# Optimization experiments

Hardware: AMD Instinct MI355X
Metric: run time of the kernel (lower is better)

## Reference

```python
import jax, jax.numpy as jnp
import numpy as np

B, N, D = 2, 4096, 1024
DS = 1024           # state_dim (defaults to embed_dim)
H = 4096            # mlp hidden = int(embed_dim * 4.0)
EPS = 1e-5


def _layernorm(x, w, b):
    mu = jnp.mean(x, axis=-1, keepdims=True)
    var = jnp.mean((x - mu) ** 2, axis=-1, keepdims=True)
    return (x - mu) * jax.lax.rsqrt(var + EPS) * w + b


def _selective_scan(deltaA, deltaB_u):
    # deltaA: (B, N, 1), deltaB_u: (B, N, DS). Recurrence h_i = dA_i * h + dBu_i.
    def step(h, inp):
        dA, dBu = inp           # (B,1), (B,DS)
        h = dA * h + dBu
        return h, h
    h0 = jnp.zeros((deltaB_u.shape[0], deltaB_u.shape[2]), deltaB_u.dtype)
    _, ys = jax.lax.scan(step, h0,
                         (jnp.swapaxes(deltaA, 0, 1), jnp.swapaxes(deltaB_u, 0, 1)))
    return jnp.swapaxes(ys, 0, 1)   # (B, N, DS)


def _forward(x, norm1_w, norm1_b, gate_w, gate_b, state_w, state_b,
             out_w, out_b, norm2_w, norm2_b, mlp_w1, mlp_b1, mlp_w2, mlp_b2):
    xn = _layernorm(x, norm1_w, norm1_b)
    g = xn @ gate_w + gate_b                       # (B,N,2D)
    gate, gate_gate = jnp.split(g, 2, axis=-1)
    gate = jax.nn.silu(gate)
    gate_gate = jax.nn.silu(gate_gate)
    u = (xn * gate) @ state_w + state_b            # (B,N,DS)
    Bm = gate_gate @ state_w + state_b             # (B,N,DS)
    # A = -ones(DS) -> delta*A = -delta broadcast over DS; keep (B,N,1)
    delta = jax.nn.softplus(jnp.mean(xn @ state_w + state_b, axis=-1, keepdims=True))
    deltaA = jnp.exp(-delta)                       # (B,N,1)
    deltaB_u = delta * Bm * u                      # (B,N,DS)
    # C = ones -> y_i = C_i * h_i = h_i
    y = _selective_scan(deltaA, deltaB_u)
    ssm_out = y @ out_w + out_b
    x = x + ssm_out
    x2 = _layernorm(x, norm2_w, norm2_b)
    mlp = jax.nn.gelu(x2 @ mlp_w1 + mlp_b1, approximate=False) @ mlp_w2 + mlp_b2
    return x + mlp


def setup_inputs() -> dict:
    key = jax.random.key(0)
    ks = jax.random.split(key, 12)
    s = 0.02
    p = lambda k, shape: jax.random.normal(k, shape, jnp.float32) * s
    return {
        "x": jax.random.normal(ks[0], (B, N, D), jnp.float32),
        "norm1_w": jnp.ones((D,), jnp.float32), "norm1_b": jnp.zeros((D,), jnp.float32),
        "gate_w": p(ks[1], (D, 2 * D)), "gate_b": p(ks[2], (2 * D,)),
        "state_w": p(ks[3], (D, DS)), "state_b": p(ks[4], (DS,)),
        "out_w": p(ks[5], (DS, D)), "out_b": p(ks[6], (D,)),
        "norm2_w": jnp.ones((D,), jnp.float32), "norm2_b": jnp.zeros((D,), jnp.float32),
        "mlp_w1": p(ks[7], (D, H)), "mlp_b1": p(ks[8], (H,)),
        "mlp_w2": p(ks[9], (H, D)), "mlp_b2": p(ks[10], (D,)),
    }


def reference(x, norm1_w, norm1_b, gate_w, gate_b, state_w, state_b,
              out_w, out_b, norm2_w, norm2_b, mlp_w1, mlp_b1, mlp_w2, mlp_b2):
    return _forward(x, norm1_w, norm1_b, gate_w, gate_b, state_w, state_b,
                    out_w, out_b, norm2_w, norm2_b, mlp_w1, mlp_b1, mlp_w2, mlp_b2)
```

## Files before the change

kernel.cpp:

```cpp
#include <hip/hip_runtime.h>
#include <hip/hip_bf16.h>
#include <math.h>

#define B_   2
#define N_   4096
#define D_   1024
#define DS_  1024
#define HID_ 4096
#define ROWS (B_ * N_)

#define CHK 128
#define TCH 32

typedef __attribute__((ext_vector_type(8))) short bf16x8;
typedef __attribute__((ext_vector_type(4))) float f32x4;

#define ASG __attribute__((address_space(1)))
#define AS3 __attribute__((address_space(3)))

__device__ __forceinline__ float bf2f(unsigned short u) {
  union { float f; unsigned int i; } v; v.i = ((unsigned int)u) << 16; return v.f;
}
__device__ __forceinline__ unsigned short f2bf(float f) {
  union { float f; unsigned int i; } v; v.f = f;
  unsigned int r = v.i + 0x7fffu + ((v.i >> 16) & 1u);
  return (unsigned short)(r >> 16);
}

__global__ void means_kernel(const float* __restrict__ W, const float* __restrict__ bvec,
                             float* __restrict__ swmean, float* __restrict__ sbmean) {
  __shared__ float sm[4];
  int bid = blockIdx.x, t = threadIdx.x;
  const float* src = (bid < D_) ? (W + (size_t)bid * DS_) : bvec;
  float s = 0.f;
  for (int j = t; j < DS_; j += 256) s += src[j];
  for (int o = 32; o; o >>= 1) s += __shfl_down(s, o);
  if ((t & 63) == 0) sm[t >> 6] = s;
  __syncthreads();
  if (t == 0) {
    float r = (sm[0] + sm[1] + sm[2] + sm[3]) * (1.f / DS_);
    if (bid < D_) swmean[bid] = r; else sbmean[0] = r;
  }
}

__global__ void transpose_all_kernel(const float* __restrict__ gw, const float* __restrict__ sw,
                                     const float* __restrict__ ow, const float* __restrict__ w1,
                                     const float* __restrict__ w2,
                                     unsigned short* __restrict__ gwT, unsigned short* __restrict__ swT,
                                     unsigned short* __restrict__ owT, unsigned short* __restrict__ w1T,
                                     unsigned short* __restrict__ w2T) {
  __shared__ float tile[32][33];
  int b = blockIdx.x;
  const float* W; unsigned short* WT; int K, N, t0;
  if (b < 2048)      { W = gw; WT = gwT; K = 1024; N = 2048; t0 = b; }
  else if (b < 3072) { W = sw; WT = swT; K = 1024; N = 1024; t0 = b - 2048; }
  else if (b < 4096) { W = ow; WT = owT; K = 1024; N = 1024; t0 = b - 3072; }
  else if (b < 8192) { W = w1; WT = w1T; K = 1024; N = 4096; t0 = b - 4096; }
  else               { W = w2; WT = w2T; K = 4096; N = 1024; t0 = b - 8192; }
  int ntx = N >> 5;
  int bn = (t0 % ntx) * 32, bk = (t0 / ntx) * 32;
  int tx = threadIdx.x & 31, ty = threadIdx.x >> 5;
  for (int i = ty; i < 32; i += 8)
    tile[i][tx] = W[(size_t)(bk + i) * N + bn + tx];
  __syncthreads();
  for (int i = ty; i < 32; i += 8)
    WT[(size_t)(bn + i) * K + bk + tx] = f2bf(tile[tx][i]);
}

template<bool WITH_DELTA, bool BF16IN>
__global__ void ln_kernel(const void* __restrict__ xin, const float* __restrict__ w,
                          const float* __restrict__ bb, unsigned short* __restrict__ out_bf,
                          const float* __restrict__ swmean, const float* __restrict__ sbmean,
                          float* __restrict__ delta, float* __restrict__ ea) {
  __shared__ float sm[8];
  __shared__ float bc[2];
  int row = blockIdx.x, t = threadIdx.x;
  float x0, x1, x2, x3;
  if (BF16IN) {
    const unsigned short* xr = (const unsigned short*)xin + (size_t)row * D_;
    ushort4 xv = ((const ushort4*)xr)[t];
    x0 = bf2f(xv.x); x1 = bf2f(xv.y); x2 = bf2f(xv.z); x3 = bf2f(xv.w);
  } else {
    const float* xr = (const float*)xin + (size_t)row * D_;
    float4 xv = ((const float4*)xr)[t];
    x0 = xv.x; x1 = xv.y; x2 = xv.z; x3 = xv.w;
  }
  float s  = x0 + x1 + x2 + x3;
  float sq = x0 * x0 + x1 * x1 + x2 * x2 + x3 * x3;
  for (int o = 32; o; o >>= 1) { s += __shfl_down(s, o); sq += __shfl_down(sq, o); }
  if ((t & 63) == 0) { sm[t >> 6] = s; sm[4 + (t >> 6)] = sq; }
  __syncthreads();
  if (t == 0) {
    float ts = sm[0] + sm[1] + sm[2] + sm[3];
    float tq = sm[4] + sm[5] + sm[6] + sm[7];
    float mu = ts * (1.f / D_);
    float var = tq * (1.f / D_) - mu * mu;
    bc[0] = mu; bc[1] = rsqrtf(var + 1e-5f);
  }
  __syncthreads();
  float mu = bc[0], rs = bc[1];
  float4 wv = ((const float4*)w)[t];
  float4 bv = ((const float4*)bb)[t];
  float n0 = (x0 - mu) * rs * wv.x + bv.x;
  float n1 = (x1 - mu) * rs * wv.y + bv.y;
  float n2 = (x2 - mu) * rs * wv.z + bv.z;
  float n3 = (x3 - mu) * rs * wv.w + bv.w;
  ushort4 o4; o4.x = f2bf(n0); o4.y = f2bf(n1); o4.z = f2bf(n2); o4.w = f2bf(n3);
  ((ushort4*)(out_bf + (size_t)row * D_))[t] = o4;
  if (WITH_DELTA) {
    float4 sw = ((const float4*)swmean)[t];
    float d = n0 * sw.x + n1 * sw.y + n2 * sw.z + n3 * sw.w;
    for (int o = 32; o; o >>= 1) d += __shfl_down(d, o);
    if ((t & 63) == 0) sm[t >> 6] = d;
    __syncthreads();
    if (t == 0) {
      float z = sm[0] + sm[1] + sm[2] + sm[3] + sbmean[0];
      float dl = (z > 15.f) ? z : log1pf(__expf(z));
      delta[row] = dl;
      ea[row] = __expf(-dl);
    }
  }
}


#define BARX { __builtin_amdgcn_s_barrier(); __builtin_amdgcn_sched_barrier(0); }

#define RD_A(TAU, H) { const char* ab_ = smem + ((((TAU)&1)*2+(H))<<14); \
  _Pragma("unroll") for (int mm_ = 0; mm_ < MB_H; ++mm_) \
  _Pragma("unroll") for (int ks_ = 0; ks_ < 2; ++ks_) { \
    int r_ = wr*(16*MB_H) + mm_*16 + l15; \
    int by_ = r_*128 + ks_*64 + kq16; by_ ^= ((by_>>7)&7)<<4; \
    af[mm_][ks_] = *(const bf16x8*)(ab_ + by_); } }

#define RD_B(TAU, H, DST) { const char* bb_ = smemB + ((((TAU)&1)*2+(H)))*SB; \
  _Pragma("unroll") for (int nn_ = 0; nn_ < NB_H; ++nn_) \
  _Pragma("unroll") for (int ks_ = 0; ks_ < 2; ++ks_) { \
    int r_ = wc*(16*NB_H) + nn_*16 + l15; \
    int by_ = r_*128 + ks_*64 + kq16; by_ ^= ((by_>>7)&7)<<4; \
    DST[nn_][ks_] = *(const bf16x8*)(bb_ + by_); } }

#define MFMAQ(QA, QB, BF) { __builtin_amdgcn_s_setprio(1); \
  _Pragma("unroll") for (int m_ = 0; m_ < MB_H; ++m_) \
  _Pragma("unroll") for (int n_ = 0; n_ < NB_H; ++n_) \
  _Pragma("unroll") for (int k_ = 0; k_ < 2; ++k_) \
    acc[(QA)*MB_H+m_][(QB)*NB_H+n_] = __builtin_amdgcn_mfma_f32_16x16x32_bf16( \
        af[m_][k_], BF[n_][k_], acc[(QA)*MB_H+m_][(QB)*NB_H+n_], 0, 0, 0); \
  __builtin_amdgcn_s_setprio(0); }

template<int EPI>
__device__ __forceinline__ void epi_store(float v, size_t off, void* Cout, const float* res) {
  if (EPI == 1) {
    v = v / (1.f + __expf(-v));
    ((unsigned short*)Cout)[off] = f2bf(v);
  } else if (EPI == 2) {
    ((unsigned short*)Cout)[off] = f2bf(v);
  } else if (EPI == 3) {
    ((float*)Cout)[off] = v + res[off];
  } else if (EPI == 4) {
    float tt = v * (0.7978845608f + 0.0356774081f * v * v);
    v = v / (1.f + __expf(-2.f * tt));
    ((unsigned short*)Cout)[off] = f2bf(v);
  } else if (EPI == 6) {
    ((unsigned short*)Cout)[off] = f2bf(v + res[off]);
  } else if (EPI == 7) {
    ((float*)Cout)[off] = v + bf2f(((const unsigned short*)res)[off]);
  }
}

template<int BN, int EPI>
__global__ __launch_bounds__(512, 2) void gemm8p(
    const unsigned short* __restrict__ A1p, int lda1, int M1,
    const unsigned short* __restrict__ A2p, int lda2,
    const unsigned short* __restrict__ BT, const float* __restrict__ bias,
    void* __restrict__ Cout, const float* __restrict__ res,
    int N, int K, int nbx) {
  constexpr int WN   = (BN == 256) ? 4 : 2;
  constexpr int MB_H = (BN == 256) ? 4 : 2;
  constexpr int NB_H = 2;
  constexpr int MF   = 2 * MB_H;
  constexpr int LB   = BN / 128;
  constexpr int SB   = (BN / 2) * 64 * 2;
  __shared__ char smem[65536 + 4 * SB];
  char* smemB = smem + 65536;

  const int nwg = gridDim.x;
  int bid = blockIdx.x;
  int wg = (bid & 7) * (nwg >> 3) + (bid >> 3);
  const int bx = wg % nbx, by = wg / nbx;
  const int mbase = by * 256, nbase = bx * BN;

  const int tid = threadIdx.x;
  const int lane = tid & 63, wid = tid >> 6;
  const int wr = wid / WN, wc = wid % WN;
  const int l15 = lane & 15, kq16 = (lane >> 4) * 16;
  const int wvoff16 = wid << 10;

  const unsigned short* Ause; int ldaU;
  if (mbase < M1) { Ause = A1p + (size_t)mbase * lda1; ldaU = lda1; }
  else            { Ause = A2p + (size_t)(mbase - M1) * lda2; ldaU = lda2; }

  int L0 = tid * 16;        int b0 = L0 ^ (((L0 >> 7) & 7) << 4);
  int L1 = 8192 + tid * 16; int b1 = L1 ^ (((L1 >> 7) & 7) << 4);
  const unsigned short* pA0 = Ause + (size_t)(b0 >> 7) * ldaU + ((b0 & 127) >> 1);
  const unsigned short* pA1 = Ause + (size_t)(b1 >> 7) * ldaU + ((b1 & 127) >> 1);
  const unsigned short* pB0 = BT + (size_t)(nbase + (b0 >> 7)) * K + ((b0 & 127) >> 1);
  const unsigned short* pB1 = BT + (size_t)(nbase + (b1 >> 7)) * K + ((b1 & 127) >> 1);

  auto stageA = [&](int tau, int h, bool en) {
    if (!en) return;
    char* l0 = smem + (((tau & 1) * 2 + h) << 14) + wvoff16;
    const unsigned short* g0 = pA0 + (size_t)h * 128 * ldaU + tau * 64;
    const unsigned short* g1 = pA1 + (size_t)h * 128 * ldaU + tau * 64;
    __builtin_amdgcn_global_load_lds((const ASG void*)g0, (AS3 void*)l0, 16, 0, 0);
    __builtin_amdgcn_global_load_lds((const ASG void*)g1, (AS3 void*)(l0 + 8192), 16, 0, 0);
  };
  auto stageB = [&](int tau, int h, bool en) {
    if (!en) return;
    char* l0 = smemB + ((tau & 1) * 2 + h) * SB + wvoff16;
    const unsigned short* g0 = pB0 + (size_t)h * (BN / 2) * K + tau * 64;
    __builtin_amdgcn_global_load_lds((const ASG void*)g0, (AS3 void*)l0, 16, 0, 0);
    if constexpr (LB == 2) {
      const unsigned short* g1 = pB1 + (size_t)h * (BN / 2) * K + tau * 64;
      __builtin_amdgcn_global_load_lds((const ASG void*)g1, (AS3 void*)(l0 + 8192), 16, 0, 0);
    }
  };
  auto vm_steady = [&]() {
    if constexpr (BN == 256) { asm volatile("s_waitcnt vmcnt(6)" ::: "memory"); }
    else                     { asm volatile("s_waitcnt vmcnt(5)" ::: "memory"); }
  };

  f32x4 acc[MF][4];
#pragma unroll
  for (int m = 0; m < MF; ++m)
#pragma unroll
    for (int n = 0; n < 4; ++n) acc[m][n] = (f32x4){0.f, 0.f, 0.f, 0.f};
  bf16x8 af[MB_H][2], bq0[NB_H][2], bq1[NB_H][2];

  const int NT = K >> 6, NI = NT >> 1;

  stageA(0, 0, true); stageB(0, 0, true); stageA(0, 1, true); stageB(0, 1, true);
  stageA(1, 0, true); stageB(1, 0, true); stageA(1, 1, true);
  vm_steady();
  BARX;

#pragma unroll 1
  for (int i = 0; i < NI; ++i) {
    const int t0 = 2 * i;
    const bool st = (i < NI - 1);
    stageB(t0 + 1, 1, true); RD_A(t0, 0); RD_B(t0, 0, bq0);
    BARX; MFMAQ(0, 0, bq0); BARX;
    stageA(t0 + 2, 0, st); RD_B(t0, 1, bq1);
    BARX; MFMAQ(0, 1, bq1); BARX;
    stageB(t0 + 2, 0, st); RD_A(t0, 1);
    BARX; MFMAQ(1, 1, bq1); BARX;
    stageA(t0 + 2, 1, st);
    if (st) { vm_steady(); } else { asm volatile("s_waitcnt vmcnt(0)" ::: "memory"); }
    BARX; MFMAQ(1, 0, bq0); BARX;
    stageB(t0 + 2, 1, st); RD_A(t0 + 1, 0); RD_B(t0 + 1, 0, bq0);
    BARX; MFMAQ(0, 0, bq0); BARX;
    stageA(t0 + 3, 0, st); RD_B(t0 + 1, 1, bq1);
    BARX; MFMAQ(0, 1, bq1); BARX;
    stageB(t0 + 3, 0, st); RD_A(t0 + 1, 1);
    BARX; MFMAQ(1, 1, bq1); BARX;
    stageA(t0 + 3, 1, st);
    if (st) vm_steady();
    BARX; MFMAQ(1, 0, bq0); BARX;
  }

  const int r0 = (lane >> 4) * 4;
#pragma unroll
  for (int mb = 0; mb < MF; ++mb) {
    int row = mbase + wr * (16 * MB_H) + (mb % MB_H) * 16 + (mb / MB_H) * 128 + r0;
#pragma unroll
    for (int nb = 0; nb < 4; ++nb) {
      int col = nbase + wc * (16 * NB_H) + (nb % NB_H) * 16 + (nb / NB_H) * (BN / 2) + l15;
      float bc = bias[col];
#pragma unroll
      for (int r = 0; r < 4; ++r)
        epi_store<EPI>(acc[mb][nb][r] + bc, (size_t)(row + r) * N + col, Cout, res);
    }
  }
}

__global__ void ew_xg_kernel(const unsigned short* __restrict__ xn,
                             const unsigned short* __restrict__ gs,
                             unsigned short* __restrict__ xg) {
  size_t i8 = ((size_t)blockIdx.x * 256 + threadIdx.x) * 8;
  size_t row = i8 >> 10, col = i8 & 1023;
  uint4 xv = *(const uint4*)(xn + i8);
  uint4 gv = *(const uint4*)(gs + row * 2048 + col);
  const unsigned short* xs = (const unsigned short*)&xv;
  const unsigned short* gg = (const unsigned short*)&gv;
  uint4 ov; unsigned short* o = (unsigned short*)&ov;
#pragma unroll
  for (int j = 0; j < 8; ++j) o[j] = f2bf(bf2f(xs[j]) * bf2f(gg[j]));
  *(uint4*)(xg + i8) = ov;
}

__global__ void scan_a_kernel(const unsigned short* __restrict__ u,
                              const unsigned short* __restrict__ bm,
                              const float* __restrict__ delta,
                              const float* __restrict__ ea,
                              float* __restrict__ hend, float* __restrict__ P) {
  int blk = blockIdx.x;
  int b = blk / CHK, c = blk % CHK;
  int ch = threadIdx.x;
  size_t base = ((size_t)(b * N_ + c * TCH)) * DS_ + ch;
  const float* dp = delta + b * N_ + c * TCH;
  const float* ep = ea + b * N_ + c * TCH;
  float h = 0.f, pa = 1.f;
#pragma unroll 4
  for (int t = 0; t < TCH; ++t) {
    float dl = dp[t], e = ep[t];
    float du = dl * bf2f(u[base + (size_t)t * DS_]) * bf2f(bm[base + (size_t)t * DS_]);
    h = e * h + du;
    pa *= e;
  }
  hend[(size_t)blk * DS_ + ch] = h;
  if (ch == 0) P[blk] = pa;
}

__global__ void scan_combine_kernel(const float* __restrict__ hend, const float* __restrict__ P,
                                    float* __restrict__ carryin) {
  int b = blockIdx.x >> 2;
  int ch = (blockIdx.x & 3) * 256 + threadIdx.x;
  float carry = 0.f;
  for (int c = 0; c < CHK; ++c) {
    size_t o = (size_t)(b * CHK + c) * DS_ + ch;
    carryin[o] = carry;
    carry = P[b * CHK + c] * carry + hend[o];
  }
}

__global__ void scan_b_kernel(const unsigned short* __restrict__ u,
                              const unsigned short* __restrict__ bm,
                              const float* __restrict__ delta,
                              const float* __restrict__ ea,
                              const float* __restrict__ carryin,
                              unsigned short* __restrict__ y) {
  int blk = blockIdx.x;
  int b = blk / CHK, c = blk % CHK;
  int ch = threadIdx.x;
  size_t base = ((size_t)(b * N_ + c * TCH)) * DS_ + ch;
  const float* dp = delta + b * N_ + c * TCH;
  const float* ep = ea + b * N_ + c * TCH;
  float h = carryin[(size_t)blk * DS_ + ch];
#pragma unroll 4
  for (int t = 0; t < TCH; ++t) {
    float dl = dp[t], e = ep[t];
    float du = dl * bf2f(u[base + (size_t)t * DS_]) * bf2f(bm[base + (size_t)t * DS_]);
    h = e * h + du;
    y[base + (size_t)t * DS_] = f2bf(h);
  }
}

extern "C" void kernel_launch(void* const* d_in, const int* in_sizes, int n_in,
                              void* d_out, int out_size, void* d_ws, size_t ws_size,
                              hipStream_t stream) {
  const float* x       = (const float*)d_in[0];
  const float* n1w     = (const float*)d_in[1];
  const float* n1b     = (const float*)d_in[2];
  const float* gate_w  = (const float*)d_in[3];
  const float* gate_b  = (const float*)d_in[4];
  const float* state_w = (const float*)d_in[5];
  const float* state_b = (const float*)d_in[6];
  const float* out_w   = (const float*)d_in[7];
  const float* out_b   = (const float*)d_in[8];
  const float* n2w     = (const float*)d_in[9];
  const float* n2b     = (const float*)d_in[10];
  const float* mlp_w1  = (const float*)d_in[11];
  const float* mlp_b1  = (const float*)d_in[12];
  const float* mlp_w2  = (const float*)d_in[13];
  const float* mlp_b2  = (const float*)d_in[14];
  float* outp = (float*)d_out;

  char* w = (char*)d_ws;
  size_t off = 0;
  auto alloc = [&](size_t bytes) { char* p = w + off; off += (bytes + 255) & ~(size_t)255; return p; };

  unsigned short* gate_wT  = (unsigned short*)alloc((size_t)2048 * 1024 * 2);
  unsigned short* state_wT = (unsigned short*)alloc((size_t)1024 * 1024 * 2);
  unsigned short* out_wT   = (unsigned short*)alloc((size_t)1024 * 1024 * 2);
  unsigned short* w1T      = (unsigned short*)alloc((size_t)4096 * 1024 * 2);
  unsigned short* w2T      = (unsigned short*)alloc((size_t)1024 * 4096 * 2);
  float* swmean  = (float*)alloc(D_ * 4);
  float* sbmean  = (float*)alloc(256);
  float* delta   = (float*)alloc((size_t)ROWS * 4);
  float* eadel   = (float*)alloc((size_t)ROWS * 4);
  float* hend    = (float*)alloc((size_t)B_ * CHK * DS_ * 4);
  float* carryin = (float*)alloc((size_t)B_ * CHK * DS_ * 4);
  float* P       = (float*)alloc((size_t)B_ * CHK * 4);
  unsigned short* xn = (unsigned short*)alloc((size_t)ROWS * D_ * 2);
  unsigned short* gs = (unsigned short*)alloc((size_t)ROWS * HID_ * 2);
  unsigned short* xg = (unsigned short*)alloc((size_t)ROWS * D_ * 2);
  float* x1f         = (float*)alloc((size_t)ROWS * D_ * 4);

  unsigned short* h1  = gs;
  unsigned short* y   = xg;
  unsigned short* x2  = xg;
  unsigned short* u   = (unsigned short*)x1f;
  unsigned short* bm  = u + (size_t)ROWS * D_;
  unsigned short* x1b = u;

  means_kernel<<<D_ + 1, 256, 0, stream>>>(state_w, state_b, swmean, sbmean);
  transpose_all_kernel<<<12288, 256, 0, stream>>>(gate_w, state_w, out_w, mlp_w1, mlp_w2,
                                                  gate_wT, state_wT, out_wT, w1T, w2T);

  ln_kernel<true, false><<<ROWS, 256, 0, stream>>>(x, n1w, n1b, xn, swmean, sbmean, delta, eadel);

  const int BIG = 1 << 30;
  gemm8p<256, 1><<<256, 512, 0, stream>>>(xn, 1024, BIG, xn, 1024,
                                          gate_wT, gate_b, gs, nullptr, 2048, 1024, 8);
  ew_xg_kernel<<<(ROWS * D_) / 8 / 256, 256, 0, stream>>>(xn, gs, xg);
  gemm8p<256, 2><<<256, 512, 0, stream>>>(xg, 1024, 8192, gs + 1024, 2048,
                                          state_wT, state_b, u, nullptr, 1024, 1024, 4);

  scan_a_kernel<<<B_ * CHK, 1024, 0, stream>>>(u, bm, delta, eadel, hend, P);
  scan_combine_kernel<<<B_ * 4, 256, 0, stream>>>(hend, P, carryin);
  scan_b_kernel<<<B_ * CHK, 1024, 0, stream>>>(u, bm, delta, eadel, carryin, y);

  gemm8p<128, 6><<<256, 512, 0, stream>>>(y, 1024, BIG, y, 1024,
                                          out_wT, out_b, x1b, x, 1024, 1024, 8);
  ln_kernel<false, true><<<ROWS, 256, 0, stream>>>(x1b, n2w, n2b, x2, nullptr, nullptr, nullptr, nullptr);
  gemm8p<256, 4><<<512, 512, 0, stream>>>(x2, 1024, BIG, x2, 1024,
                                          w1T, mlp_b1, h1, nullptr, 4096, 1024, 16);
  gemm8p<128, 7><<<256, 512, 0, stream>>>(h1, 4096, BIG, h1, 4096,
                                          w2T, mlp_b2, outp, (const float*)x1b, 1024, 4096, 8);
}
```

Baseline: 351.1 us.

## Fuse delta*Bm*u into state GEMM epilogue via interleaved row layout

The gate GEMM epilogue now applies SiLU and writes gate_gate directly into odd rows of an interleaved A buffer, while the elementwise kernel writes xn*gate into the even rows. The state GEMM then runs over this interleaved 2*ROWS matrix, and its epilogue pairs adjacent rows to emit delta*u*Bm straight as a bf16 tensor. The scan kernels read one precomputed tensor instead of u, Bm and delta, which removes a full read stream and the separate u/Bm stores. This relies on each thread's four accumulator rows being consecutive and aligned so that row pairs land in the same thread. Precision changes slightly because the product is rounded to bf16 before the scan.

```diff
diff --git a/kernel.cpp b/kernel.cpp
--- a/kernel.cpp
+++ b/kernel.cpp
@@ -173,7 +173,7 @@
     const unsigned short* __restrict__ A2p, int lda2,
     const unsigned short* __restrict__ BT, const float* __restrict__ bias,
     void* __restrict__ Cout, const float* __restrict__ res,
-    int N, int K, int nbx) {
+    int N, int K, int nbx, void* __restrict__ Cout2) {
   constexpr int WN   = (BN == 256) ? 4 : 2;
   constexpr int MB_H = (BN == 256) ? 4 : 2;
   constexpr int NB_H = 2;
@@ -275,45 +275,61 @@
     for (int nb = 0; nb < 4; ++nb) {
       int col = nbase + wc * (16 * NB_H) + (nb % NB_H) * 16 + (nb / NB_H) * (BN / 2) + l15;
       float bc = bias[col];
-#pragma unroll
-      for (int r = 0; r < 4; ++r)
-        epi_store<EPI>(acc[mb][nb][r] + bc, (size_t)(row + r) * N + col, Cout, res);
+      if (EPI == 9) {
+#pragma unroll
+        for (int pr = 0; pr < 2; ++pr) {
+          float e0 = acc[mb][nb][2 * pr] + bc;
+          float e1 = acc[mb][nb][2 * pr + 1] + bc;
+          int i0 = (row >> 1) + pr;
+          ((unsigned short*)Cout)[(size_t)i0 * N + col] = f2bf(res[i0] * e0 * e1);
+        }
+      } else if (EPI == 8) {
+#pragma unroll
+        for (int r = 0; r < 4; ++r) {
+          float v = acc[mb][nb][r] + bc;
+          v = v / (1.f + __expf(-v));
+          if (col < 1024)
+            ((unsigned short*)Cout)[(size_t)(row + r) * 1024 + col] = f2bf(v);
+          else
+            ((unsigned short*)Cout2)[(size_t)(2 * (row + r) + 1) * 1024 + (col - 1024)] = f2bf(v);
+        }
+      } else {
+#pragma unroll
+        for (int r = 0; r < 4; ++r)
+          epi_store<EPI>(acc[mb][nb][r] + bc, (size_t)(row + r) * N + col, Cout, res);
+      }
     }
   }
 }
 
 __global__ void ew_xg_kernel(const unsigned short* __restrict__ xn,
-                             const unsigned short* __restrict__ gs,
-                             unsigned short* __restrict__ xg) {
+                             const unsigned short* __restrict__ gs1,
+                             unsigned short* __restrict__ AI) {
   size_t i8 = ((size_t)blockIdx.x * 256 + threadIdx.x) * 8;
   size_t row = i8 >> 10, col = i8 & 1023;
   uint4 xv = *(const uint4*)(xn + i8);
-  uint4 gv = *(const uint4*)(gs + row * 2048 + col);
+  uint4 gv = *(const uint4*)(gs1 + i8);
   const unsigned short* xs = (const unsigned short*)&xv;
   const unsigned short* gg = (const unsigned short*)&gv;
   uint4 ov; unsigned short* o = (unsigned short*)&ov;
 #pragma unroll
   for (int j = 0; j < 8; ++j) o[j] = f2bf(bf2f(xs[j]) * bf2f(gg[j]));
-  *(uint4*)(xg + i8) = ov;
-}
-
-__global__ void scan_a_kernel(const unsigned short* __restrict__ u,
-                              const unsigned short* __restrict__ bm,
-                              const float* __restrict__ delta,
+  *(uint4*)(AI + ((row * 2) << 10) + col) = ov;
+}
+
+__global__ void scan_a_kernel(const unsigned short* __restrict__ dbu,
                               const float* __restrict__ ea,
                               float* __restrict__ hend, float* __restrict__ P) {
   int blk = blockIdx.x;
   int b = blk / CHK, c = blk % CHK;
   int ch = threadIdx.x;
   size_t base = ((size_t)(b * N_ + c * TCH)) * DS_ + ch;
-  const float* dp = delta + b * N_ + c * TCH;
   const float* ep = ea + b * N_ + c * TCH;
   float h = 0.f, pa = 1.f;
 #pragma unroll 4
   for (int t = 0; t < TCH; ++t) {
-    float dl = dp[t], e = ep[t];
-    float du = dl * bf2f(u[base + (size_t)t * DS_]) * bf2f(bm[base + (size_t)t * DS_]);
-    h = e * h + du;
+    float e = ep[t];
+    h = e * h + bf2f(dbu[base + (size_t)t * DS_]);
     pa *= e;
   }
   hend[(size_t)blk * DS_ + ch] = h;
@@ -332,9 +348,7 @@
   }
 }
 
-__global__ void scan_b_kernel(const unsigned short* __restrict__ u,
-                              const unsigned short* __restrict__ bm,
-                              const float* __restrict__ delta,
+__global__ void scan_b_kernel(const unsigned short* __restrict__ dbu,
                               const float* __restrict__ ea,
                               const float* __restrict__ carryin,
                               unsigned short* __restrict__ y) {
@@ -342,14 +356,12 @@
   int b = blk / CHK, c = blk % CHK;
   int ch = threadIdx.x;
   size_t base = ((size_t)(b * N_ + c * TCH)) * DS_ + ch;
-  const float* dp = delta + b * N_ + c * TCH;
   const float* ep = ea + b * N_ + c * TCH;
   float h = carryin[(size_t)blk * DS_ + ch];
 #pragma unroll 4
   for (int t = 0; t < TCH; ++t) {
-    float dl = dp[t], e = ep[t];
-    float du = dl * bf2f(u[base + (size_t)t * DS_]) * bf2f(bm[base + (size_t)t * DS_]);
-    h = e * h + du;
+    float e = ep[t];
+    h = e * h + bf2f(dbu[base + (size_t)t * DS_]);
     y[base + (size_t)t * DS_] = f2bf(h);
   }
 }
@@ -392,15 +404,15 @@
   float* P       = (float*)alloc((size_t)B_ * CHK * 4);
   unsigned short* xn = (unsigned short*)alloc((size_t)ROWS * D_ * 2);
   unsigned short* gs = (unsigned short*)alloc((size_t)ROWS * HID_ * 2);
-  unsigned short* xg = (unsigned short*)alloc((size_t)ROWS * D_ * 2);
-  float* x1f         = (float*)alloc((size_t)ROWS * D_ * 4);
-
+  unsigned short* yx = (unsigned short*)alloc((size_t)ROWS * D_ * 2);
+  unsigned short* AI = (unsigned short*)alloc((size_t)2 * ROWS * D_ * 2);
+
+  unsigned short* dbu = xn;
+  unsigned short* gs1 = gs;
   unsigned short* h1  = gs;
-  unsigned short* y   = xg;
-  unsigned short* x2  = xg;
-  unsigned short* u   = (unsigned short*)x1f;
-  unsigned short* bm  = u + (size_t)ROWS * D_;
-  unsigned short* x1b = u;
+  unsigned short* y   = yx;
+  unsigned short* x2  = yx;
+  unsigned short* x1b = AI;
 
   means_kernel<<<D_ + 1, 256, 0, stream>>>(state_w, state_b, swmean, sbmean);
   transpose_all_kernel<<<12288, 256, 0, stream>>>(gate_w, state_w, out_w, mlp_w1, mlp_w2,
@@ -409,21 +421,21 @@
   ln_kernel<true, false><<<ROWS, 256, 0, stream>>>(x, n1w, n1b, xn, swmean, sbmean, delta, eadel);
 
   const int BIG = 1 << 30;
-  gemm8p<256, 1><<<256, 512, 0, stream>>>(xn, 1024, BIG, xn, 1024,
-                                          gate_wT, gate_b, gs, nullptr, 2048, 1024, 8);
-  ew_xg_kernel<<<(ROWS * D_) / 8 / 256, 256, 0, stream>>>(xn, gs, xg);
-  gemm8p<256, 2><<<256, 512, 0, stream>>>(xg, 1024, 8192, gs + 1024, 2048,
-                                          state_wT, state_b, u, nullptr, 1024, 1024, 4);
-
-  scan_a_kernel<<<B_ * CHK, 1024, 0, stream>>>(u, bm, delta, eadel, hend, P);
+  gemm8p<256, 8><<<256, 512, 0, stream>>>(xn, 1024, BIG, xn, 1024,
+                                          gate_wT, gate_b, gs1, nullptr, 2048, 1024, 8, AI);
+  ew_xg_kernel<<<(ROWS * D_) / 8 / 256, 256, 0, stream>>>(xn, gs1, AI);
+  gemm8p<256, 9><<<256, 512, 0, stream>>>(AI, 1024, BIG, AI, 1024,
+                                          state_wT, state_b, dbu, delta, 1024, 1024, 4, nullptr);
+
+  scan_a_kernel<<<B_ * CHK, 1024, 0, stream>>>(dbu, eadel, hend, P);
   scan_combine_kernel<<<B_ * 4, 256, 0, stream>>>(hend, P, carryin);
-  scan_b_kernel<<<B_ * CHK, 1024, 0, stream>>>(u, bm, delta, eadel, carryin, y);
+  scan_b_kernel<<<B_ * CHK, 1024, 0, stream>>>(dbu, eadel, carryin, y);
 
   gemm8p<128, 6><<<256, 512, 0, stream>>>(y, 1024, BIG, y, 1024,
-                                          out_wT, out_b, x1b, x, 1024, 1024, 8);
+                                          out_wT, out_b, x1b, x, 1024, 1024, 8, nullptr);
   ln_kernel<false, true><<<ROWS, 256, 0, stream>>>(x1b, n2w, n2b, x2, nullptr, nullptr, nullptr, nullptr);
   gemm8p<256, 4><<<512, 512, 0, stream>>>(x2, 1024, BIG, x2, 1024,
-                                          w1T, mlp_b1, h1, nullptr, 4096, 1024, 16);
+                                          w1T, mlp_b1, h1, nullptr, 4096, 1024, 16, nullptr);
   gemm8p<128, 7><<<256, 512, 0, stream>>>(h1, 4096, BIG, h1, 4096,
-                                          w2T, mlp_b2, outp, (const float*)x1b, 1024, 4096, 8);
-}
+                                          w2T, mlp_b2, outp, (const float*)x1b, 1024, 4096, 8, nullptr);
+}
```

After: 350.6 us. No clear change (-0.1%).
